# Kernel optimization log

Hardware: AMD Instinct MI355X
Metric: run time of the kernel (lower is better)

Reference implementation:

```python
import jax, jax.numpy as jnp
import numpy as np

CUTOFF = 5.0
N_GAUSS = 25
LOG2 = 0.6931471805599453
N_INTER = 3


def ssp(x):
    # shifted softplus used by SchNet
    return jax.nn.softplus(x) - LOG2


def setup_inputs() -> dict:
    key = jax.random.key(0)
    ks = jax.random.split(key, 16)
    B, A, N, F, G, Z = 16, 128, 127, 128, N_GAUSS, 100
    s = 1.0 / np.sqrt(F)
    emb = jax.random.normal(ks[0], (Z, F), jnp.float32)
    emb = emb.at[0].set(0.0)  # padding_idx=0
    inp = {
        "positions": jax.random.normal(ks[1], (B, A, 3), jnp.float32) * 3.0,
        "cell": jnp.zeros((B, 3, 3), jnp.float32),
        "cell_offset": jnp.zeros((B, A, N, 3), jnp.float32),
        "neighbor_mask": jnp.ones((B, A, N), jnp.float32),
        "embeddings": emb,
        "filt_W1": jax.random.normal(ks[2], (N_INTER, G, F), jnp.float32) / np.sqrt(G),
        "filt_b1": jnp.zeros((N_INTER, F), jnp.float32),
        "filt_W2": jax.random.normal(ks[3], (N_INTER, F, F), jnp.float32) * s,
        "filt_b2": jnp.zeros((N_INTER, F), jnp.float32),
        "in2f_W": jax.random.normal(ks[4], (N_INTER, F, F), jnp.float32) * s,
        "f2out_W": jax.random.normal(ks[5], (N_INTER, F, F), jnp.float32) * s,
        "f2out_b": jnp.zeros((N_INTER, F), jnp.float32),
        "dense_W": jax.random.normal(ks[6], (N_INTER, F, F), jnp.float32) * s,
        "dense_b": jnp.zeros((N_INTER, F), jnp.float32),
        "atomic_numbers": jax.random.randint(ks[7], (B, A), 1, Z).astype(jnp.int32),
        "neighbors": jax.random.randint(ks[8], (B, A, N), 0, A).astype(jnp.int32),
    }
    return inp


def _schnet_forward(positions, cell, cell_offset, neighbor_mask, embeddings,
                    filt_W1, filt_b1, filt_W2, filt_b2,
                    in2f_W, f2out_W, f2out_b, dense_W, dense_b,
                    atomic_numbers, neighbors):
    B, A, _ = positions.shape
    bidx = jnp.arange(B)[:, None, None]

    # ---- AtomDistances: gather neighbor positions, pairwise distances ----
    pos_nbh = positions[bidx, neighbors]            # [B,A,N,3]
    dvec = pos_nbh - positions[:, :, None, :]
    dvec = dvec + jnp.einsum('banj,bjc->banc', cell_offset, cell)
    d2 = jnp.sum(dvec * dvec, axis=-1)              # [B,A,N]
    m = neighbor_mask > 0
    r_ij = jnp.where(m, jnp.sqrt(jnp.where(m, d2, 1.0)), 0.0)

    # ---- GaussianSmearing(0, cutoff, 25) ----
    centers = jnp.linspace(0.0, CUTOFF, N_GAUSS, dtype=r_ij.dtype)
    width = centers[1] - centers[0]
    coeff = -0.5 / (width * width)
    diff = r_ij[..., None] - centers                # [B,A,N,G]
    f_ij = jnp.exp(coeff * diff * diff)

    # ---- CosineCutoff ----
    C = 0.5 * (jnp.cos(r_ij * jnp.pi / CUTOFF) + 1.0)
    C = C * (r_ij < CUTOFF).astype(r_ij.dtype)      # [B,A,N]

    # ---- embedding ----
    x = embeddings[atomic_numbers]                  # [B,A,F]

    # ---- interaction blocks (cfconv + dense residual) ----
    for l in range(N_INTER):
        W = ssp(jnp.einsum('bang,gf->banf', f_ij, filt_W1[l]) + filt_b1[l])
        W = jnp.einsum('banf,fg->bang', W, filt_W2[l]) + filt_b2[l]
        W = W * C[..., None]                        # [B,A,N,F]
        y = x @ in2f_W[l]                           # [B,A,F], no bias
        y_nbh = y[bidx, neighbors]                  # [B,A,N,F]
        agg = jnp.sum(y_nbh * W * neighbor_mask[..., None], axis=2)  # [B,A,F]
        v = ssp(agg @ f2out_W[l] + f2out_b[l])
        v = v @ dense_W[l] + dense_b[l]
        x = x + v
    return x


def reference(positions, cell, cell_offset, neighbor_mask, embeddings,
              filt_W1, filt_b1, filt_W2, filt_b2,
              in2f_W, f2out_W, f2out_b, dense_W, dense_b,
              atomic_numbers, neighbors):
    return _schnet_forward(positions, cell, cell_offset, neighbor_mask, embeddings,
                           filt_W1, filt_b1, filt_W2, filt_b2,
                           in2f_W, f2out_W, f2out_b, dense_W, dense_b,
                           atomic_numbers, neighbors)
```

## Files before the change

### kernel.cpp

```cpp
#include <hip/hip_runtime.h>
#include <math.h>

#define BB 16
#define AA 128
#define NNB 127
#define FF 128
#define GG 25

typedef __attribute__((ext_vector_type(8))) short bf16x8;
typedef __attribute__((ext_vector_type(4))) float f32x4;
typedef unsigned short ushort_t;

__device__ __forceinline__ float ssp_f(float x) {
    return fmaxf(x, 0.f) + log1pf(__expf(-fabsf(x))) - 0.6931471805599453f;
}

__device__ __forceinline__ float ssp_fast(float x) {
    float e = __expf(-fabsf(x));
    float p = fmaf(e, 0.03215845f, -0.13606275f);
    p = fmaf(e, p, 0.28947478f);
    p = fmaf(e, p, -0.49190896f);
    p = fmaf(e, p, 0.99949556f);
    return fmaxf(x, 0.f) + e * p - 0.6931471805599453f;
}

__device__ __forceinline__ ushort_t f2bf(float f) {
    unsigned int u = __float_as_uint(f);
    unsigned int r = (u + 0x7fffu + ((u >> 16) & 1u)) >> 16;
    return (ushort_t)r;
}

__device__ __forceinline__ float bf2f(ushort_t h) {
    return __uint_as_float(((unsigned int)h) << 16);
}

__device__ __forceinline__ unsigned int pack2bf(float lo, float hi) {
    return (unsigned int)f2bf(lo) | ((unsigned int)f2bf(hi) << 16);
}

__global__ __launch_bounds__(256) void k_prep(const float* __restrict__ W1,
                                              const float* __restrict__ W2,
                                              const float* __restrict__ Win,
                                              const float* __restrict__ Wf,
                                              const float* __restrict__ Wd,
                                              ushort_t* __restrict__ w1t,
                                              ushort_t* __restrict__ w2f,
                                              ushort_t* __restrict__ whi,
                                              ushort_t* __restrict__ wlo) {
    int i = blockIdx.x * 256 + threadIdx.x;
    if (i < 3 * 128 * 32) {
        int l = i >> 12, rem = i & 4095, f = rem >> 5, g = rem & 31;
        float v = (g < GG) ? W1[l * GG * FF + g * FF + f] : 0.f;
        w1t[i] = f2bf(v);
    }
    if (i < 3 * 16384) {
        int l = i >> 14, e = i & 16383;
        int u = e >> 3, j = e & 7;
        int ks = u >> 9, rem = u & 511;
        int wcft = rem >> 6, lane = rem & 63;
        int f = (wcft >> 1) * 32 + (wcft & 1) * 16 + (lane & 15);
        int k = ks * 32 + (lane >> 4) * 8 + j;
        w2f[i] = f2bf(W2[l * 16384 + k * 128 + f]);
    }
    if (i < 9 * 16384) {
        int m = i / 49152;
        int rem = i - m * 49152;
        int l = rem >> 14;
        int rk = rem & 16383;
        int f = rk >> 7, k = rk & 127;
        const float* src = (m == 0) ? Win : ((m == 1) ? Wf : Wd);
        float v = src[l * 16384 + k * 128 + f];
        ushort_t h = f2bf(v);
        whi[i] = h;
        wlo[i] = f2bf(v - bf2f(h));
    }
}

__global__ __launch_bounds__(256) void k_init_x(const float* __restrict__ emb,
                                                const int* __restrict__ z,
                                                float* __restrict__ x) {
    int i = blockIdx.x * 256 + threadIdx.x;
    if (i < BB * AA * FF) {
        int row = i >> 7, f = i & 127;
        x[i] = emb[z[row] * FF + f];
    }
}

__global__ __launch_bounds__(512) void k_ffn(
    const float* __restrict__ agg, const float* __restrict__ x_in,
    float* __restrict__ x_out, float* __restrict__ y, float* __restrict__ out,
    const ushort_t* __restrict__ wfh, const ushort_t* __restrict__ wfl, const float* __restrict__ bfv_g,
    const ushort_t* __restrict__ wdh, const ushort_t* __restrict__ wdl, const float* __restrict__ bdv_g,
    const ushort_t* __restrict__ wih, const ushort_t* __restrict__ wil,
    int mode) {
    __shared__ ushort_t tsh[8][136];
    __shared__ ushort_t tsl[8][136];
    const int t = threadIdx.x;
    const int lane = t & 63, w = t >> 6;
    const int l15 = lane & 15, l4 = lane >> 4;
    const int r0 = blockIdx.x << 3;
    const int fcol = (w << 4) + l15;

    bf16x8 Ah[4], Al[4];

    auto loadA_global = [&](const float* __restrict__ M) {
#pragma unroll
        for (int ks = 0; ks < 4; ++ks) {
            float v[8];
            if (l15 < 8) {
                const float4* p = (const float4*)(M + ((size_t)(r0 + l15) << 7) + (ks << 5) + (l4 << 3));
                float4 a = p[0], b = p[1];
                v[0] = a.x; v[1] = a.y; v[2] = a.z; v[3] = a.w;
                v[4] = b.x; v[5] = b.y; v[6] = b.z; v[7] = b.w;
            } else {
#pragma unroll
                for (int j = 0; j < 8; ++j) v[j] = 0.f;
            }
#pragma unroll
            for (int j = 0; j < 8; ++j) {
                ushort_t h = f2bf(v[j]);
                Ah[ks][j] = (short)h;
                Al[ks][j] = (short)f2bf(v[j] - bf2f(h));
            }
        }
    };
    auto loadA_lds = [&]() {
#pragma unroll
        for (int ks = 0; ks < 4; ++ks) {
            if (l15 < 8) {
                const char* base = (const char*)&tsh[l15][0] + (ks << 6) + (l4 << 4);
                Ah[ks] = *(const bf16x8*)base;
                const char* basel = (const char*)&tsl[l15][0] + (ks << 6) + (l4 << 4);
                Al[ks] = *(const bf16x8*)basel;
            } else {
#pragma unroll
                for (int j = 0; j < 8; ++j) { Ah[ks][j] = 0; Al[ks][j] = 0; }
            }
        }
    };

    if (mode & 1) {
        loadA_global(agg);
        float bfv = bfv_g[fcol];
        f32x4 acc = {bfv, bfv, bfv, bfv};
#pragma unroll
        for (int ks = 0; ks < 4; ++ks) {
            const bf16x8 Bh = *(const bf16x8*)(wfh + ((size_t)fcol << 7) + (ks << 5) + (l4 << 3));
            const bf16x8 Bl = *(const bf16x8*)(wfl + ((size_t)fcol << 7) + (ks << 5) + (l4 << 3));
            acc = __builtin_amdgcn_mfma_f32_16x16x32_bf16(Al[ks], Bh, acc, 0, 0, 0);
            acc = __builtin_amdgcn_mfma_f32_16x16x32_bf16(Ah[ks], Bl, acc, 0, 0, 0);
            acc = __builtin_amdgcn_mfma_f32_16x16x32_bf16(Ah[ks], Bh, acc, 0, 0, 0);
        }
#pragma unroll
        for (int reg = 0; reg < 4; ++reg) {
            int r = (l4 << 2) + reg;
            if (r < 8) {
                float v = ssp_f(acc[reg]);
                ushort_t h = f2bf(v);
                tsh[r][fcol] = h;
                tsl[r][fcol] = f2bf(v - bf2f(h));
            }
        }
        __syncthreads();
        loadA_lds();
        float bdv = bdv_g[fcol];
        f32x4 acc2 = {bdv, bdv, bdv, bdv};
#pragma unroll
        for (int ks = 0; ks < 4; ++ks) {
            const bf16x8 Bh = *(const bf16x8*)(wdh + ((size_t)fcol << 7) + (ks << 5) + (l4 << 3));
            const bf16x8 Bl = *(const bf16x8*)(wdl + ((size_t)fcol << 7) + (ks << 5) + (l4 << 3));
            acc2 = __builtin_amdgcn_mfma_f32_16x16x32_bf16(Al[ks], Bh, acc2, 0, 0, 0);
            acc2 = __builtin_amdgcn_mfma_f32_16x16x32_bf16(Ah[ks], Bl, acc2, 0, 0, 0);
            acc2 = __builtin_amdgcn_mfma_f32_16x16x32_bf16(Ah[ks], Bh, acc2, 0, 0, 0);
        }
        __syncthreads();
#pragma unroll
        for (int reg = 0; reg < 4; ++reg) {
            int r = (l4 << 2) + reg;
            if (r < 8) {
                size_t gi = ((size_t)(r0 + r) << 7) + fcol;
                float xn = x_in[gi] + acc2[reg];
                x_out[gi] = xn;
                if (mode & 4) out[gi] = xn;
                if (mode & 2) {
                    ushort_t h = f2bf(xn);
                    tsh[r][fcol] = h;
                    tsl[r][fcol] = f2bf(xn - bf2f(h));
                }
            }
        }
        if (mode & 2) __syncthreads();
    }
    if (mode & 2) {
        if (mode & 1) loadA_lds(); else loadA_global(x_in);
        f32x4 acc3 = {0.f, 0.f, 0.f, 0.f};
#pragma unroll
        for (int ks = 0; ks < 4; ++ks) {
            const bf16x8 Bh = *(const bf16x8*)(wih + ((size_t)fcol << 7) + (ks << 5) + (l4 << 3));
            const bf16x8 Bl = *(const bf16x8*)(wil + ((size_t)fcol << 7) + (ks << 5) + (l4 << 3));
            acc3 = __builtin_amdgcn_mfma_f32_16x16x32_bf16(Al[ks], Bh, acc3, 0, 0, 0);
            acc3 = __builtin_amdgcn_mfma_f32_16x16x32_bf16(Ah[ks], Bl, acc3, 0, 0, 0);
            acc3 = __builtin_amdgcn_mfma_f32_16x16x32_bf16(Ah[ks], Bh, acc3, 0, 0, 0);
        }
#pragma unroll
        for (int reg = 0; reg < 4; ++reg) {
            int r = (l4 << 2) + reg;
            if (r < 8) y[((size_t)(r0 + r) << 7) + fcol] = acc3[reg];
        }
    }
}

#define SMEM_BYTES 34304

__global__ __launch_bounds__(512, 6) void k_cfconv(
    const float* __restrict__ positions, const float* __restrict__ cell,
    const float* __restrict__ cell_offset, const float* __restrict__ nmask,
    const int* __restrict__ neighbors,
    const ushort_t* __restrict__ w1t, const float* __restrict__ b1,
    const ushort_t* __restrict__ w2f, const float* __restrict__ b2,
    const float* __restrict__ y, float* __restrict__ agg) {
    extern __shared__ char smem[];
    float* cm_s = (float*)(smem + 32768);
    int* nbr_s = (int*)(smem + 33280);
    float* r_s = (float*)(smem + 33792);
    float* red_s = (float*)smem;

    const int row = blockIdx.x;
    const int b = row >> 7;
    const int t = threadIdx.x;
    const int lane = t & 63, w = t >> 6;
    const int l15 = lane & 15, l4 = lane >> 4;
    const int wr = w >> 2, wc = w & 3;

    if (t < NNB) {
        int nb = neighbors[row * NNB + t];
        nbr_s[t] = nb;
        float px = positions[row * 3 + 0], py = positions[row * 3 + 1], pz = positions[row * 3 + 2];
        int nrow = b * AA + nb;
        float qx = positions[nrow * 3 + 0], qy = positions[nrow * 3 + 1], qz = positions[nrow * 3 + 2];
        const float* co = cell_offset + (size_t)row * NNB * 3 + (size_t)t * 3;
        const float* cl = cell + b * 9;
        float c0 = co[0], c1 = co[1], c2 = co[2];
        float ox = c0 * cl[0] + c1 * cl[3] + c2 * cl[6];
        float oy = c0 * cl[1] + c1 * cl[4] + c2 * cl[7];
        float oz = c0 * cl[2] + c1 * cl[5] + c2 * cl[8];
        float dx = qx - px + ox, dy = qy - py + oy, dz = qz - pz + oz;
        float d2 = dx * dx + dy * dy + dz * dz;
        float mk = nmask[row * NNB + t];
        float r = (mk > 0.f) ? sqrtf(d2) : 0.f;
        r_s[t] = r;
        float Cc = 0.5f * (__cosf(r * (3.14159265358979323846f / 5.0f)) + 1.f);
        Cc = (r < 5.0f) ? Cc : 0.f;
        cm_s[t] = Cc * mk;
    } else if (t == NNB) {
        cm_s[NNB] = 0.f; nbr_s[NNB] = 0; r_s[NNB] = 1e9f;
    }
    __syncthreads();

    {
        const int nrow = (w << 4) + l15;
        const float rv = r_s[nrow];
        const float width = 5.0f / (GG - 1);
        const float coeff = -0.5f / (width * width);
        bf16x8 fb;
#pragma unroll
        for (int j = 0; j < 8; ++j) {
            int g = (l4 << 3) + j;
            float d = rv - g * width;
            float v = (g < GG && nrow < NNB) ? __expf(coeff * d * d) : 0.f;
            fb[j] = (short)f2bf(v);
        }
        const int base = nrow * 256;
        const int sw = (nrow & 7) << 4;
#pragma unroll
        for (int ft = 0; ft < 8; ++ft) {
            bf16x8 aw = *(const bf16x8*)(w1t + ((ft << 4) + l15) * 32 + (l4 << 3));
            const int f0 = (ft << 4) + (l4 << 2);
            f32x4 c0 = *(const f32x4*)(b1 + f0);
            f32x4 d = __builtin_amdgcn_mfma_f32_16x16x32_bf16(aw, fb, c0, 0, 0, 0);
            unsigned long long pk =
                (unsigned long long)pack2bf(ssp_fast(d[0]), ssp_fast(d[1])) |
                ((unsigned long long)pack2bf(ssp_fast(d[2]), ssp_fast(d[3])) << 32);
            *(unsigned long long*)(smem + base + ((f0 << 1) ^ sw)) = pk;
        }
    }

#define W2LD(ks, ft) (*(const bf16x8*)(w2f + (((((ks) << 3) + (wc << 1) + (ft)) << 6) + lane) * 8))
    bf16x8 wb0 = W2LD(0, 0), wb1 = W2LD(0, 1);
    __syncthreads();

    f32x4 acc[4][2];
#pragma unroll
    for (int mi = 0; mi < 4; ++mi)
#pragma unroll
        for (int ft = 0; ft < 2; ++ft) {
            float b2v = b2[(wc << 5) + (ft << 4) + l15];
            f32x4 c0 = {b2v, b2v, b2v, b2v};
            acc[mi][ft] = c0;
        }
#pragma unroll
    for (int ks = 0; ks < 4; ++ks) {
        bf16x8 wn0, wn1;
        if (ks < 3) { wn0 = W2LD(ks + 1, 0); wn1 = W2LD(ks + 1, 1); }
        bf16x8 ha[4];
#pragma unroll
        for (int mi = 0; mi < 4; ++mi) {
            int n = (wr << 6) + (mi << 4) + l15;
            ha[mi] = *(const bf16x8*)(smem + n * 256 + ((((ks << 2) + l4) << 4) ^ ((n & 7) << 4)));
        }
#pragma unroll
        for (int mi = 0; mi < 4; ++mi) {
            acc[mi][0] = __builtin_amdgcn_mfma_f32_16x16x32_bf16(ha[mi], wb0, acc[mi][0], 0, 0, 0);
            acc[mi][1] = __builtin_amdgcn_mfma_f32_16x16x32_bf16(ha[mi], wb1, acc[mi][1], 0, 0, 0);
        }
        if (ks < 3) { wb0 = wn0; wb1 = wn1; }
    }
#undef W2LD
    __syncthreads();

    float part0 = 0.f, part1 = 0.f;
    const float* ybase = y + ((size_t)(b * AA) << 7) + (wc << 5) + l15;
#pragma unroll
    for (int mi = 0; mi < 4; ++mi) {
        float yv0[4], yv1[4], cmv[4];
#pragma unroll
        for (int r = 0; r < 4; ++r) {
            int n = (wr << 6) + (mi << 4) + (l4 << 2) + r;
            int nb = nbr_s[n];
            cmv[r] = cm_s[n];
            const float* yr = ybase + ((size_t)nb << 7);
            yv0[r] = yr[0];
            yv1[r] = yr[16];
        }
#pragma unroll
        for (int r = 0; r < 4; ++r) {
            part0 = fmaf(yv0[r], acc[mi][0][r] * cmv[r], part0);
            part1 = fmaf(yv1[r], acc[mi][1][r] * cmv[r], part1);
        }
    }
    {
        int xg = l4 << 3;
        red_s[(w << 7) + (l4 << 5) + (l15 ^ xg)] = part0;
        red_s[(w << 7) + (l4 << 5) + ((16 + l15) ^ xg)] = part1;
    }
    __syncthreads();
    if (t < FF) {
        int wcf = t >> 5, fl = t & 31;
        float s = 0.f;
#pragma unroll
        for (int wr2 = 0; wr2 < 2; ++wr2)
#pragma unroll
            for (int g = 0; g < 4; ++g)
                s += red_s[(((wr2 << 2) + wcf) << 7) + (g << 5) + (fl ^ (g << 3))];
        agg[(size_t)row * FF + t] = s;
    }
}

extern "C" void kernel_launch(void* const* d_in, const int* in_sizes, int n_in,
                              void* d_out, int out_size, void* d_ws, size_t ws_size,
                              hipStream_t stream) {
    const float* positions   = (const float*)d_in[0];
    const float* cell        = (const float*)d_in[1];
    const float* cell_offset = (const float*)d_in[2];
    const float* nmask       = (const float*)d_in[3];
    const float* emb         = (const float*)d_in[4];
    const float* filt_W1     = (const float*)d_in[5];
    const float* filt_b1     = (const float*)d_in[6];
    const float* filt_W2     = (const float*)d_in[7];
    const float* filt_b2     = (const float*)d_in[8];
    const float* in2f_W      = (const float*)d_in[9];
    const float* f2out_W     = (const float*)d_in[10];
    const float* f2out_b     = (const float*)d_in[11];
    const float* dense_W     = (const float*)d_in[12];
    const float* dense_b     = (const float*)d_in[13];
    const int* atomic_numbers = (const int*)d_in[14];
    const int* neighbors      = (const int*)d_in[15];
    float* out = (float*)d_out;

    float* x   = (float*)d_ws;
    float* yb  = x + BB * AA * FF;
    float* agg = yb + BB * AA * FF;
    ushort_t* w1t = (ushort_t*)(agg + BB * AA * FF);
    ushort_t* w2f = w1t + 3 * 128 * 32;
    ushort_t* whi = w2f + 3 * 16384;
    ushort_t* wlo = whi + 9 * 16384;

    k_prep<<<576, 256, 0, stream>>>(filt_W1, filt_W2, in2f_W, f2out_W, dense_W,
                                    w1t, w2f, whi, wlo);
    k_init_x<<<(BB * AA * FF + 255) / 256, 256, 0, stream>>>(emb, atomic_numbers, x);

    k_ffn<<<256, 512, 0, stream>>>(x, x, x, yb, out,
                                   whi + 3 * 16384, wlo + 3 * 16384, f2out_b,
                                   whi + 6 * 16384, wlo + 6 * 16384, dense_b,
                                   whi + 0 * 16384, wlo + 0 * 16384,
                                   2);
    for (int l = 0; l < 3; ++l) {
        k_cfconv<<<BB * AA, 512, SMEM_BYTES, stream>>>(
            positions, cell, cell_offset, nmask, neighbors,
            w1t + (size_t)l * 128 * 32, filt_b1 + (size_t)l * FF,
            w2f + (size_t)l * 16384, filt_b2 + (size_t)l * FF,
            yb, agg);
        int nextl = (l < 2) ? (l + 1) : 0;
        int mode = 1 | ((l < 2) ? 2 : 0) | ((l == 2) ? 4 : 0);
        k_ffn<<<256, 512, 0, stream>>>(agg, x, x, yb, out,
                                       whi + (3 + l) * 16384, wlo + (3 + l) * 16384, f2out_b + (size_t)l * FF,
                                       whi + (6 + l) * 16384, wlo + (6 + l) * 16384, dense_b + (size_t)l * FF,
                                       whi + nextl * 16384, wlo + nextl * 16384,
                                       mode);
    }
}
```

Before: 127.5 us.

## Fuse per-atom FFN and next-layer projection into cfconv epilogue

Removes the separate k_ffn kernel and the bf16 hi/lo weight split. Each cfconv block now runs the f2out, dense residual and next in2f matvecs for its own atom row in fp32 CUDA-core code, with weights read straight from global memory. A small k_y kernel computes the first projection, and y is double-buffered so a layer's cfconv can write the next y while other blocks still read the current one. This saves kernel launches and agg round trips, but every one of the 2048 blocks now re-reads three 64KB weight matrices through cache and does scalar matvecs instead of MFMA.

```diff
diff --git a/kernel.cpp b/kernel.cpp
--- a/kernel.cpp
+++ b/kernel.cpp
@@ -30,23 +30,14 @@
     return (ushort_t)r;
 }
 
-__device__ __forceinline__ float bf2f(ushort_t h) {
-    return __uint_as_float(((unsigned int)h) << 16);
-}
-
 __device__ __forceinline__ unsigned int pack2bf(float lo, float hi) {
     return (unsigned int)f2bf(lo) | ((unsigned int)f2bf(hi) << 16);
 }
 
 __global__ __launch_bounds__(256) void k_prep(const float* __restrict__ W1,
                                               const float* __restrict__ W2,
-                                              const float* __restrict__ Win,
-                                              const float* __restrict__ Wf,
-                                              const float* __restrict__ Wd,
                                               ushort_t* __restrict__ w1t,
-                                              ushort_t* __restrict__ w2f,
-                                              ushort_t* __restrict__ whi,
-                                              ushort_t* __restrict__ wlo) {
+                                              ushort_t* __restrict__ w2f) {
     int i = blockIdx.x * 256 + threadIdx.x;
     if (i < 3 * 128 * 32) {
         int l = i >> 12, rem = i & 4095, f = rem >> 5, g = rem & 31;
@@ -62,18 +53,6 @@
         int k = ks * 32 + (lane >> 4) * 8 + j;
         w2f[i] = f2bf(W2[l * 16384 + k * 128 + f]);
     }
-    if (i < 9 * 16384) {
-        int m = i / 49152;
-        int rem = i - m * 49152;
-        int l = rem >> 14;
-        int rk = rem & 16383;
-        int f = rk >> 7, k = rk & 127;
-        const float* src = (m == 0) ? Win : ((m == 1) ? Wf : Wd);
-        float v = src[l * 16384 + k * 128 + f];
-        ushort_t h = f2bf(v);
-        whi[i] = h;
-        wlo[i] = f2bf(v - bf2f(h));
-    }
 }
 
 __global__ __launch_bounds__(256) void k_init_x(const float* __restrict__ emb,
@@ -86,128 +65,25 @@
     }
 }
 
-__global__ __launch_bounds__(512) void k_ffn(
-    const float* __restrict__ agg, const float* __restrict__ x_in,
-    float* __restrict__ x_out, float* __restrict__ y, float* __restrict__ out,
-    const ushort_t* __restrict__ wfh, const ushort_t* __restrict__ wfl, const float* __restrict__ bfv_g,
-    const ushort_t* __restrict__ wdh, const ushort_t* __restrict__ wdl, const float* __restrict__ bdv_g,
-    const ushort_t* __restrict__ wih, const ushort_t* __restrict__ wil,
-    int mode) {
-    __shared__ ushort_t tsh[8][136];
-    __shared__ ushort_t tsl[8][136];
-    const int t = threadIdx.x;
-    const int lane = t & 63, w = t >> 6;
-    const int l15 = lane & 15, l4 = lane >> 4;
-    const int r0 = blockIdx.x << 3;
-    const int fcol = (w << 4) + l15;
-
-    bf16x8 Ah[4], Al[4];
-
-    auto loadA_global = [&](const float* __restrict__ M) {
-#pragma unroll
-        for (int ks = 0; ks < 4; ++ks) {
-            float v[8];
-            if (l15 < 8) {
-                const float4* p = (const float4*)(M + ((size_t)(r0 + l15) << 7) + (ks << 5) + (l4 << 3));
-                float4 a = p[0], b = p[1];
-                v[0] = a.x; v[1] = a.y; v[2] = a.z; v[3] = a.w;
-                v[4] = b.x; v[5] = b.y; v[6] = b.z; v[7] = b.w;
-            } else {
-#pragma unroll
-                for (int j = 0; j < 8; ++j) v[j] = 0.f;
-            }
-#pragma unroll
-            for (int j = 0; j < 8; ++j) {
-                ushort_t h = f2bf(v[j]);
-                Ah[ks][j] = (short)h;
-                Al[ks][j] = (short)f2bf(v[j] - bf2f(h));
-            }
-        }
-    };
-    auto loadA_lds = [&]() {
-#pragma unroll
-        for (int ks = 0; ks < 4; ++ks) {
-            if (l15 < 8) {
-                const char* base = (const char*)&tsh[l15][0] + (ks << 6) + (l4 << 4);
-                Ah[ks] = *(const bf16x8*)base;
-                const char* basel = (const char*)&tsl[l15][0] + (ks << 6) + (l4 << 4);
-                Al[ks] = *(const bf16x8*)basel;
-            } else {
-#pragma unroll
-                for (int j = 0; j < 8; ++j) { Ah[ks][j] = 0; Al[ks][j] = 0; }
-            }
-        }
-    };
-
-    if (mode & 1) {
-        loadA_global(agg);
-        float bfv = bfv_g[fcol];
-        f32x4 acc = {bfv, bfv, bfv, bfv};
-#pragma unroll
-        for (int ks = 0; ks < 4; ++ks) {
-            const bf16x8 Bh = *(const bf16x8*)(wfh + ((size_t)fcol << 7) + (ks << 5) + (l4 << 3));
-            const bf16x8 Bl = *(const bf16x8*)(wfl + ((size_t)fcol << 7) + (ks << 5) + (l4 << 3));
-            acc = __builtin_amdgcn_mfma_f32_16x16x32_bf16(Al[ks], Bh, acc, 0, 0, 0);
-            acc = __builtin_amdgcn_mfma_f32_16x16x32_bf16(Ah[ks], Bl, acc, 0, 0, 0);
-            acc = __builtin_amdgcn_mfma_f32_16x16x32_bf16(Ah[ks], Bh, acc, 0, 0, 0);
-        }
-#pragma unroll
-        for (int reg = 0; reg < 4; ++reg) {
-            int r = (l4 << 2) + reg;
-            if (r < 8) {
-                float v = ssp_f(acc[reg]);
-                ushort_t h = f2bf(v);
-                tsh[r][fcol] = h;
-                tsl[r][fcol] = f2bf(v - bf2f(h));
-            }
-        }
-        __syncthreads();
-        loadA_lds();
-        float bdv = bdv_g[fcol];
-        f32x4 acc2 = {bdv, bdv, bdv, bdv};
-#pragma unroll
-        for (int ks = 0; ks < 4; ++ks) {
-            const bf16x8 Bh = *(const bf16x8*)(wdh + ((size_t)fcol << 7) + (ks << 5) + (l4 << 3));
-            const bf16x8 Bl = *(const bf16x8*)(wdl + ((size_t)fcol << 7) + (ks << 5) + (l4 << 3));
-            acc2 = __builtin_amdgcn_mfma_f32_16x16x32_bf16(Al[ks], Bh, acc2, 0, 0, 0);
-            acc2 = __builtin_amdgcn_mfma_f32_16x16x32_bf16(Ah[ks], Bl, acc2, 0, 0, 0);
-            acc2 = __builtin_amdgcn_mfma_f32_16x16x32_bf16(Ah[ks], Bh, acc2, 0, 0, 0);
-        }
-        __syncthreads();
-#pragma unroll
-        for (int reg = 0; reg < 4; ++reg) {
-            int r = (l4 << 2) + reg;
-            if (r < 8) {
-                size_t gi = ((size_t)(r0 + r) << 7) + fcol;
-                float xn = x_in[gi] + acc2[reg];
-                x_out[gi] = xn;
-                if (mode & 4) out[gi] = xn;
-                if (mode & 2) {
-                    ushort_t h = f2bf(xn);
-                    tsh[r][fcol] = h;
-                    tsl[r][fcol] = f2bf(xn - bf2f(h));
-                }
-            }
-        }
-        if (mode & 2) __syncthreads();
-    }
-    if (mode & 2) {
-        if (mode & 1) loadA_lds(); else loadA_global(x_in);
-        f32x4 acc3 = {0.f, 0.f, 0.f, 0.f};
-#pragma unroll
-        for (int ks = 0; ks < 4; ++ks) {
-            const bf16x8 Bh = *(const bf16x8*)(wih + ((size_t)fcol << 7) + (ks << 5) + (l4 << 3));
-            const bf16x8 Bl = *(const bf16x8*)(wil + ((size_t)fcol << 7) + (ks << 5) + (l4 << 3));
-            acc3 = __builtin_amdgcn_mfma_f32_16x16x32_bf16(Al[ks], Bh, acc3, 0, 0, 0);
-            acc3 = __builtin_amdgcn_mfma_f32_16x16x32_bf16(Ah[ks], Bl, acc3, 0, 0, 0);
-            acc3 = __builtin_amdgcn_mfma_f32_16x16x32_bf16(Ah[ks], Bh, acc3, 0, 0, 0);
-        }
-#pragma unroll
-        for (int reg = 0; reg < 4; ++reg) {
-            int r = (l4 << 2) + reg;
-            if (r < 8) y[((size_t)(r0 + r) << 7) + fcol] = acc3[reg];
-        }
-    }
+__global__ __launch_bounds__(128) void k_y(const float* __restrict__ x,
+                                           const float* __restrict__ W,
+                                           float* __restrict__ y) {
+    int row0 = blockIdx.x << 2, t = threadIdx.x;
+    __shared__ float xs[4][FF];
+#pragma unroll
+    for (int r = 0; r < 4; ++r) xs[r][t] = x[(row0 + r) * FF + t];
+    __syncthreads();
+    float acc[4] = {0.f, 0.f, 0.f, 0.f};
+#pragma unroll 4
+    for (int k = 0; k < FF; ++k) {
+        float wv = W[k * FF + t];
+        acc[0] = fmaf(xs[0][k], wv, acc[0]);
+        acc[1] = fmaf(xs[1][k], wv, acc[1]);
+        acc[2] = fmaf(xs[2][k], wv, acc[2]);
+        acc[3] = fmaf(xs[3][k], wv, acc[3]);
+    }
+#pragma unroll
+    for (int r = 0; r < 4; ++r) y[(row0 + r) * FF + t] = acc[r];
 }
 
 #define SMEM_BYTES 34304
@@ -218,12 +94,21 @@
     const int* __restrict__ neighbors,
     const ushort_t* __restrict__ w1t, const float* __restrict__ b1,
     const ushort_t* __restrict__ w2f, const float* __restrict__ b2,
-    const float* __restrict__ y, float* __restrict__ agg) {
+    const float* __restrict__ y,
+    float* __restrict__ x_io,
+    const float* __restrict__ Wf_g, const float* __restrict__ bf_g,
+    const float* __restrict__ Wd_g, const float* __restrict__ bd_g,
+    const float* __restrict__ win_g,
+    float* __restrict__ y_out,
+    float* __restrict__ outp, int wout) {
     extern __shared__ char smem[];
     float* cm_s = (float*)(smem + 32768);
     int* nbr_s = (int*)(smem + 33280);
     float* r_s = (float*)(smem + 33792);
     float* red_s = (float*)smem;
+    float* agg_s = (float*)(smem + 4096);
+    float* ts_s = (float*)(smem + 4608);
+    float* xn_s = (float*)(smem + 5120);
 
     const int row = blockIdx.x;
     const int b = row >> 7;
@@ -352,7 +237,54 @@
 #pragma unroll
             for (int g = 0; g < 4; ++g)
                 s += red_s[(((wr2 << 2) + wcf) << 7) + (g << 5) + (fl ^ (g << 3))];
-        agg[(size_t)row * FF + t] = s;
+        agg_s[t] = s;
+    }
+    __syncthreads();
+
+    const int f = (w << 4) + l15;
+    {
+        float p = 0.f;
+        const float* Wcol = Wf_g + f;
+#pragma unroll 8
+        for (int i = 0; i < 32; ++i) {
+            int k = (i << 2) + l4;
+            p = fmaf(agg_s[k], Wcol[(size_t)k << 7], p);
+        }
+        p += __shfl_xor(p, 16);
+        p += __shfl_xor(p, 32);
+        if (l4 == 0) ts_s[f] = ssp_f(p + bf_g[f]);
+    }
+    __syncthreads();
+    {
+        float p = 0.f;
+        const float* Wcol = Wd_g + f;
+#pragma unroll 8
+        for (int i = 0; i < 32; ++i) {
+            int k = (i << 2) + l4;
+            p = fmaf(ts_s[k], Wcol[(size_t)k << 7], p);
+        }
+        p += __shfl_xor(p, 16);
+        p += __shfl_xor(p, 32);
+        if (l4 == 0) {
+            size_t gi = ((size_t)row << 7) + f;
+            float xn = x_io[gi] + p + bd_g[f];
+            x_io[gi] = xn;
+            if (wout) outp[gi] = xn;
+            xn_s[f] = xn;
+        }
+    }
+    if (win_g) {
+        __syncthreads();
+        float p = 0.f;
+        const float* Wcol = win_g + f;
+#pragma unroll 8
+        for (int i = 0; i < 32; ++i) {
+            int k = (i << 2) + l4;
+            p = fmaf(xn_s[k], Wcol[(size_t)k << 7], p);
+        }
+        p += __shfl_xor(p, 16);
+        p += __shfl_xor(p, 32);
+        if (l4 == 0) y_out[((size_t)row << 7) + f] = p;
     }
 }
 
@@ -377,35 +309,29 @@
     const int* neighbors      = (const int*)d_in[15];
     float* out = (float*)d_out;
 
-    float* x   = (float*)d_ws;
-    float* yb  = x + BB * AA * FF;
-    float* agg = yb + BB * AA * FF;
-    ushort_t* w1t = (ushort_t*)(agg + BB * AA * FF);
+    float* x    = (float*)d_ws;
+    float* yb0  = x + BB * AA * FF;
+    float* yb1  = yb0 + BB * AA * FF;
+    ushort_t* w1t = (ushort_t*)(yb1 + BB * AA * FF);
     ushort_t* w2f = w1t + 3 * 128 * 32;
-    ushort_t* whi = w2f + 3 * 16384;
-    ushort_t* wlo = whi + 9 * 16384;
-
-    k_prep<<<576, 256, 0, stream>>>(filt_W1, filt_W2, in2f_W, f2out_W, dense_W,
-                                    w1t, w2f, whi, wlo);
+
+    k_prep<<<192, 256, 0, stream>>>(filt_W1, filt_W2, w1t, w2f);
     k_init_x<<<(BB * AA * FF + 255) / 256, 256, 0, stream>>>(emb, atomic_numbers, x);
-
-    k_ffn<<<256, 512, 0, stream>>>(x, x, x, yb, out,
-                                   whi + 3 * 16384, wlo + 3 * 16384, f2out_b,
-                                   whi + 6 * 16384, wlo + 6 * 16384, dense_b,
-                                   whi + 0 * 16384, wlo + 0 * 16384,
-                                   2);
+    k_y<<<BB * AA / 4, FF, 0, stream>>>(x, in2f_W, yb0);
+
+    float* ybufs[2] = {yb0, yb1};
     for (int l = 0; l < 3; ++l) {
+        const float* yin = ybufs[l & 1];
+        float* yout = ybufs[(l + 1) & 1];
+        const float* win = (l < 2) ? (in2f_W + (size_t)(l + 1) * FF * FF) : nullptr;
         k_cfconv<<<BB * AA, 512, SMEM_BYTES, stream>>>(
             positions, cell, cell_offset, nmask, neighbors,
             w1t + (size_t)l * 128 * 32, filt_b1 + (size_t)l * FF,
             w2f + (size_t)l * 16384, filt_b2 + (size_t)l * FF,
-            yb, agg);
-        int nextl = (l < 2) ? (l + 1) : 0;
-        int mode = 1 | ((l < 2) ? 2 : 0) | ((l == 2) ? 4 : 0);
-        k_ffn<<<256, 512, 0, stream>>>(agg, x, x, yb, out,
-                                       whi + (3 + l) * 16384, wlo + (3 + l) * 16384, f2out_b + (size_t)l * FF,
-                                       whi + (6 + l) * 16384, wlo + (6 + l) * 16384, dense_b + (size_t)l * FF,
-                                       whi + nextl * 16384, wlo + nextl * 16384,
-                                       mode);
-    }
-}
+            yin,
+            x,
+            f2out_W + (size_t)l * FF * FF, f2out_b + (size_t)l * FF,
+            dense_W + (size_t)l * FF * FF, dense_b + (size_t)l * FF,
+            win, yout, out, (l == 2) ? 1 : 0);
+    }
+}
```

After: 140.6 us. 10.3% more time.
